# Optimization experiments

Hardware: AMD Instinct MI355X
Metric: run time of the kernel (lower is better)

## Reference

```python
import jax, jax.numpy as jnp
import numpy as np

WIDTH = 1024
NH = 16
HD = 64
MBS = 16
B = 4
L = 2048
BASE_LR = 1.0
EPS = 1e-6


def gelu_tanh(x):
    return jax.nn.gelu(x, approximate=True)


def gelu_bwd(x):
    t = jnp.tanh(0.79788456 * x * (1 + 0.044715 * x * x))
    return 0.5 * x * ((1 - t * t) * (0.79788456 + 0.1070322243 * x * x)) + 0.5 * (1 + t)


def ln_fwd(x, g, b):
    mu = x.mean(-1, keepdims=True)
    var = ((x - mu) ** 2).mean(-1, keepdims=True)
    return g * ((x - mu) * jax.lax.rsqrt(var + EPS)) + b


def ln_l2_bwd(x, tgt, g, b):
    # grad of 0.5*||LN(x)-tgt||^2 wrt x
    mu = x.mean(-1, keepdims=True)
    var = ((x - mu) ** 2).mean(-1, keepdims=True)
    std = jnp.sqrt(var + EPS)
    xh = (x - mu) / std
    gx = (g * xh + b - tgt) * g
    return (gx - gx.mean(-1, keepdims=True) - xh * (gx * xh).mean(-1, keepdims=True)) / std


def adapter_forward(hidden_states, Wq, Wk, Wv, Wo, Wg, lr_w, lr_b,
                    learnable_token_idx, norm_w, norm_b, W1, b1, W2, b2,
                    post_w, post_b):
    Bb, Ll, width = hidden_states.shape
    nh, hd = norm_w.shape
    mbs = learnable_token_idx.shape[0]
    nc = Ll // mbs  # L chosen divisible by mini_batch_size

    def split_heads(x):  # [B,L,width] -> [B,nh,nc,mbs,hd]
        return x.reshape(Bb, Ll, nh, hd).transpose(0, 2, 1, 3).reshape(Bb, nh, nc, mbs, hd)

    XQ = split_heads(hidden_states @ Wq.T)
    XK = split_heads(hidden_states @ Wk.T)
    XV = split_heads(hidden_states @ Wv.T)

    # eta: learnable per-token lr gate (get_eta)
    X = hidden_states.reshape(Bb, nc, mbs, width)
    lr = jnp.einsum('bnkc,hdc->bhnkd', X, lr_w) + lr_b.reshape(1, nh, 1, 1, 1)
    lr = jax.nn.sigmoid(lr).transpose(0, 1, 2, 4, 3)  # [B,nh,nc,1,mbs]
    lr_eta = BASE_LR * lr / hd
    token_idx = jnp.clip(1.0 / jnp.arange(1, mbs + 1, dtype=hidden_states.dtype)
                         + learnable_token_idx, 0.0, None)
    token_eta = token_idx.reshape(1, 1, 1, mbs, 1)
    eta = token_eta * lr_eta  # [B,nh,nc,mbs,mbs]

    tril = jnp.tril(jnp.ones((mbs, mbs), dtype=hidden_states.dtype))
    lnw = norm_w.reshape(nh, 1, hd)
    lnb = norm_b.reshape(nh, 1, hd)

    def step(carry, xs):
        W1s, b1s, W2s, b2s = carry  # [B,nh,hd,4hd], [B,nh,1,4hd], [B,nh,4hd,hd], [B,nh,1,hd]
        XQm, XKm, XVm, etam = xs    # [B,nh,mbs,hd] x3, [B,nh,mbs,mbs]
        X1 = XKm
        Z1 = X1 @ W1s + b1s
        X2 = gelu_tanh(Z1)
        Z2 = X2 @ W2s + b2s
        gZ2 = ln_l2_bwd(Z2, XVm - XKm, lnw, lnb)
        gZ1 = (gZ2 @ jnp.swapaxes(W2s, -1, -2)) * gelu_bwd(Z1)
        eta_tril = etam * tril
        Attn1 = tril * (XQm @ jnp.swapaxes(X1, -1, -2))
        b1_bar = b1s - eta_tril @ gZ1
        Z1_bar = XQm @ W1s - (etam * Attn1) @ gZ1 + b1_bar
        X2_bar = gelu_tanh(Z1_bar)
        Attn2 = tril * (X2_bar @ jnp.swapaxes(X2, -1, -2))
        b2_bar = b2s - eta_tril @ gZ2
        Z2_bar = X2_bar @ W2s - (etam * Attn2) @ gZ2 + b2_bar
        last = etam[:, :, -1, :, None]  # [B,nh,mbs,1]
        W1n = W1s - jnp.swapaxes(last * X1, -1, -2) @ gZ1
        b1n = b1s - (last * gZ1).sum(-2, keepdims=True)
        W2n = W2s - jnp.swapaxes(last * X2, -1, -2) @ gZ2
        b2n = b2s - (last * gZ2).sum(-2, keepdims=True)
        XQW = XQm + ln_fwd(Z2_bar, lnw, lnb)
        return (W1n, b1n, W2n, b2n), XQW

    carry0 = (jnp.broadcast_to(W1, (Bb,) + W1.shape),
              jnp.broadcast_to(b1, (Bb,) + b1.shape),
              jnp.broadcast_to(W2, (Bb,) + W2.shape),
              jnp.broadcast_to(b2, (Bb,) + b2.shape))
    xs = tuple(jnp.moveaxis(t, 2, 0) for t in (XQ, XK, XV, eta))
    _, XQW = jax.lax.scan(step, carry0, xs)  # [nc,B,nh,mbs,hd]
    out = XQW.transpose(1, 0, 3, 2, 4).reshape(Bb, Ll, width)

    # post_norm (LayerNorm eps=1e-6)
    out = ln_fwd(out, post_w, post_b)
    # gate
    out = gelu_tanh(hidden_states @ Wg.T) * out
    # o_proj
    return out @ Wo.T


def setup_inputs():
    key = jax.random.key(0)
    ks = jax.random.split(key, 10)
    n = lambda k, s: jax.random.normal(k, s, dtype=jnp.float32) * 0.02
    return {
        'hidden_states': jax.random.normal(ks[0], (B, L, WIDTH), dtype=jnp.float32),
        'Wq': n(ks[1], (WIDTH, WIDTH)),
        'Wk': n(ks[2], (WIDTH, WIDTH)),
        'Wv': n(ks[3], (WIDTH, WIDTH)),
        'Wo': n(ks[4], (WIDTH, WIDTH)),
        'Wg': n(ks[5], (WIDTH, WIDTH)),
        'lr_w': n(ks[6], (NH, 1, WIDTH)),
        'lr_b': jnp.zeros((NH, 1), jnp.float32),
        'learnable_token_idx': jnp.zeros((MBS,), jnp.float32),
        'norm_w': jnp.ones((NH, HD), jnp.float32),
        'norm_b': jnp.zeros((NH, HD), jnp.float32),
        'W1': n(ks[7], (NH, HD, 4 * HD)),
        'b1': jnp.zeros((NH, 1, 4 * HD), jnp.float32),
        'W2': n(ks[8], (NH, 4 * HD, HD)),
        'b2': jnp.zeros((NH, 1, HD), jnp.float32),
        'post_w': jnp.ones((WIDTH,), jnp.float32),
        'post_b': jnp.zeros((WIDTH,), jnp.float32),
    }


def reference(hidden_states, Wq, Wk, Wv, Wo, Wg, lr_w, lr_b, learnable_token_idx,
              norm_w, norm_b, W1, b1, W2, b2, post_w, post_b):
    return adapter_forward(hidden_states, Wq, Wk, Wv, Wo, Wg, lr_w, lr_b,
                           learnable_token_idx, norm_w, norm_b, W1, b1, W2, b2,
                           post_w, post_b)
```

## Files before the change

### kernel.cpp

```cpp
#include <hip/hip_runtime.h>

#define WIDTH 1024
#define MBSZ 16
#define LLL 2048
#define NCHUNK 128

typedef __attribute__((ext_vector_type(4))) float f32x4;
typedef __attribute__((ext_vector_type(2))) float f32x2;
typedef __attribute__((ext_vector_type(8))) short short8;
typedef __attribute__((ext_vector_type(4))) short short4v;
typedef __attribute__((ext_vector_type(2))) unsigned u32x2;
typedef __attribute__((ext_vector_type(4))) unsigned u32x4;

#define MFMA16(a, b, c) __builtin_amdgcn_mfma_f32_16x16x32_bf16((a), (b), (c), 0, 0, 0)

__device__ __forceinline__ short f2bf(float f) {
  unsigned u = __float_as_uint(f);
  u = (u + 0x7FFFu + ((u >> 16) & 1u)) >> 16;
  return (short)u;
}
__device__ __forceinline__ float bf2f(short s) {
  return __uint_as_float(((unsigned)(unsigned short)s) << 16);
}
__device__ __forceinline__ unsigned cvt_pk(float lo, float hi) {
  unsigned r;
  asm("v_cvt_pk_bf16_f32 %0, %1, %2" : "=v"(r) : "v"(lo), "v"(hi));
  return r;
}
__device__ __forceinline__ float fast_e2u(float x) {
  return __builtin_amdgcn_exp2f(x * (2.30220776f + 0.10294322f * x * x));
}
__device__ __forceinline__ float gelu_f(float x) {
  float e = fast_e2u(x);
  return x * (1.0f - __builtin_amdgcn_rcpf(e + 1.0f));
}
__device__ __forceinline__ float gelu_bwd_f(float x) {
  float e = fast_e2u(x);
  float r = __builtin_amdgcn_rcpf(e + 1.0f);
  return 2.0f * x * r * (1.0f - r) * (0.79788456f + 0.1070322243f * x * x) + (1.0f - r);
}
__device__ __forceinline__ int w2row(int d) { return d * 264 + (d >> 3) * 24; }

__global__ __launch_bounds__(256) void cvt_kernel(const float* __restrict__ hs,
                                                  const float* __restrict__ Wq,
                                                  const float* __restrict__ Wk,
                                                  const float* __restrict__ Wv,
                                                  const float* __restrict__ Wg,
                                                  const float* __restrict__ Wo,
                                                  short* __restrict__ dst) {
  const long idx = ((long)blockIdx.x * 256 + threadIdx.x) * 8;
  if (idx >= 13631488L) return;
  const float* src;
  long off;
  if (idx < 8388608L)       { src = hs; off = idx; }
  else if (idx < 9437184L)  { src = Wq; off = idx - 8388608L; }
  else if (idx < 10485760L) { src = Wk; off = idx - 9437184L; }
  else if (idx < 11534336L) { src = Wv; off = idx - 10485760L; }
  else if (idx < 12582912L) { src = Wg; off = idx - 11534336L; }
  else                      { src = Wo; off = idx - 12582912L; }
  const f32x4 a = *(const f32x4*)(src + off);
  const f32x4 b = *(const f32x4*)(src + off + 4);
  u32x4 o;
  o[0] = cvt_pk(a[0], a[1]); o[1] = cvt_pk(a[2], a[3]);
  o[2] = cvt_pk(b[0], b[1]); o[3] = cvt_pk(b[2], b[3]);
  *(u32x4*)(dst + idx) = o;
}

template <int OUTBF>
__global__ __launch_bounds__(256) void gemm_bt_b(const short* __restrict__ A,
                                                 const short* __restrict__ W,
                                                 float* __restrict__ C,
                                                 short* __restrict__ Cb) {
  __shared__ __align__(16) short sA[64][40];
  __shared__ __align__(16) short sB[64][40];
  const int tid = threadIdx.x;
  const int m0 = blockIdx.x * 64, n0 = blockIdx.y * 64;
  const int srow = tid >> 2, sk = (tid & 3) * 8;
  const int wv = tid >> 6, ln = tid & 63;
  const int fr = ln & 15, kh = (ln >> 4) * 8;
  f32x4 acc[4];
#pragma unroll
  for (int s = 0; s < 4; ++s) acc[s] = (f32x4){0.f, 0.f, 0.f, 0.f};
  const short* ga = A + (long)(m0 + srow) * 1024 + sk;
  const short* gw = W + (long)(n0 + srow) * 1024 + sk;
  for (int k0 = 0; k0 < 1024; k0 += 32) {
    const short8 a8 = *(const short8*)(ga + k0);
    const short8 w8 = *(const short8*)(gw + k0);
    *(short8*)&sA[srow][sk] = a8;
    *(short8*)&sB[srow][sk] = w8;
    __syncthreads();
    short8 af = *(const short8*)&sA[wv * 16 + fr][kh];
#pragma unroll
    for (int s = 0; s < 4; ++s) {
      short8 bf8 = *(const short8*)&sB[s * 16 + fr][kh];
      acc[s] = MFMA16(af, bf8, acc[s]);
    }
    __syncthreads();
  }
  const int orow = m0 + wv * 16 + (ln >> 4) * 4;
#pragma unroll
  for (int s = 0; s < 4; ++s)
#pragma unroll
    for (int q = 0; q < 4; ++q) {
      if (OUTBF)
        Cb[(long)(orow + q) * 1024 + n0 + s * 16 + fr] = f2bf(acc[s][q]);
      else
        C[(long)(orow + q) * 1024 + n0 + s * 16 + fr] = acc[s][q];
    }
}

__global__ __launch_bounds__(256) void lr_kernel(const float* __restrict__ hs,
                                                 const float* __restrict__ lrw,
                                                 const float* __restrict__ lrb,
                                                 float* __restrict__ out) {
  __shared__ __align__(16) float row[1024];
  const int t = blockIdx.x, tid = threadIdx.x;
  *(f32x4*)&row[tid * 4] = *(const f32x4*)&hs[(long)t * 1024 + tid * 4];
  __syncthreads();
  const int hh = tid >> 4, j = tid & 15;
  const float* wrow = lrw + hh * 1024;
  float s = 0.f;
#pragma unroll 4
  for (int m = 0; m < 16; ++m) {
    const int c = j * 4 + m * 64;
    f32x4 x = *(const f32x4*)&row[c];
    f32x4 w = *(const f32x4*)&wrow[c];
    s += x[0] * w[0] + x[1] * w[1] + x[2] * w[2] + x[3] * w[3];
  }
#pragma unroll
  for (int o = 8; o; o >>= 1) s += __shfl_xor(s, o, 16);
  if (j == 0) {
    const float v = s + lrb[hh];
    const float sg = 1.f / (1.f + expf(-v));
    const int b = t >> 11, tr = t & 2047;
    out[((b << 4) + hh) * 2048 + tr] = sg * (1.f / 64.f);
  }
}

__global__ __launch_bounds__(512, 2) void scan_kernel(
    float* __restrict__ Qb, const float* __restrict__ Kb, const float* __restrict__ Vb,
    const float* __restrict__ LRb, const float* __restrict__ lti,
    const float* __restrict__ nw, const float* __restrict__ nb,
    const float* __restrict__ W1in, const float* __restrict__ b1in,
    const float* __restrict__ W2in, const float* __restrict__ b2in) {
  __shared__ __align__(16) short sW1b[256 * 72];
  __shared__ __align__(16) short sW2dp[64 * 264 + 192];
  __shared__ __align__(16) short la1T[64 * 24];
  __shared__ __align__(16) short la2T[256 * 24];
  __shared__ __align__(16) short sX1b[16 * 72];
  __shared__ __align__(16) short sXQb[16 * 72];
  __shared__ __align__(16) float sXQf[16 * 68];
  __shared__ __align__(16) float sTg[16 * 72];
  __shared__ __align__(16) short sX2b[16 * 264];
  __shared__ __align__(16) short sXbb[16 * 264];
  __shared__ __align__(16) short sG1c[256 * 24];
  __shared__ __align__(16) short sG2b[16 * 72];
  __shared__ __align__(16) short sG2c[64 * 24];
  __shared__ __align__(16) float sZ2f[16 * 68];
  __shared__ __align__(16) short sC1b[16 * 24];
  __shared__ __align__(16) short sC2b[16 * 24];
  __shared__ __align__(16) float sB1[256];
  __shared__ __align__(16) float sB2[64];
  __shared__ float sLr[16];
  __shared__ float sTok[16];
  __shared__ __align__(16) float sLnw[64];
  __shared__ __align__(16) float sLnb[64];

  const int bh = blockIdx.x, b = bh >> 4, h = bh & 15;
  const int tid = threadIdx.x;
  const int w = tid >> 6, ln = tid & 63;
  const int fr = ln & 15, half = ln >> 4, hk = half * 8;
  const int nt0 = 2 * w;

  float w1m[8][4], w2m[8][4];
#pragma unroll
  for (int r = 0; r < 8; ++r) {
    const int T = w * 8 + r, dt = T >> 4, pt = T & 15;
#pragma unroll
    for (int qq = 0; qq < 4; ++qq) {
      w1m[r][qq] = W1in[h * 16384 + (dt * 16 + half * 4 + qq) * 256 + pt * 16 + fr];
      w2m[r][qq] = W2in[h * 16384 + (pt * 16 + half * 4 + qq) * 64 + dt * 16 + fr];
    }
  }
  for (int e = tid; e < 16384; e += 512) {
    {
      const int d = e >> 8, p = e & 255;
      sW1b[p * 72 + d] = f2bf(W1in[h * 16384 + e]);
    }
    {
      const int p = e >> 6, d = e & 63;
      sW2dp[w2row(d) + (p ^ (((d >> 3) & 3) << 3))] = f2bf(W2in[h * 16384 + e]);
    }
  }
  if (tid < 256) sB1[tid] = b1in[h * 256 + tid];
  if (tid < 64) { sB2[tid] = b2in[h * 64 + tid]; sLnw[tid] = nw[h * 64 + tid]; sLnb[tid] = nb[h * 64 + tid]; }
  if (tid < 16) sTok[tid] = fmaxf(1.0f / (float)(tid + 1) + lti[tid], 0.0f);

  const f32x4 zf4 = (f32x4){0.f, 0.f, 0.f, 0.f};
  short8 zs8;
#pragma unroll
  for (int j = 0; j < 8; ++j) zs8[j] = 0;

  const int pf_i = tid >> 5;
  const int pf_d = (tid & 31) * 2;
  f32x2 pk, pq, pv;
  float plr = 0.f;
  {
    const long a0 = ((long)(b * LLL + pf_i)) * WIDTH + h * 64 + pf_d;
    pk = *(const f32x2*)&Kb[a0];
    pq = *(const f32x2*)&Qb[a0];
    pv = *(const f32x2*)&Vb[a0];
    if (tid < 16) plr = LRb[(long)bh * 2048 + tid];
  }

  for (int n = 0; n < NCHUNK; ++n) {
    const long gbase = ((long)(b * LLL + n * MBSZ)) * WIDTH + h * 64;

    {
      *(unsigned*)&sX1b[pf_i * 72 + pf_d] = cvt_pk(pk[0], pk[1]);
      *(unsigned*)&sXQb[pf_i * 72 + pf_d] = cvt_pk(pq[0], pq[1]);
      sXQf[pf_i * 68 + pf_d] = pq[0];
      sXQf[pf_i * 68 + pf_d + 1] = pq[1];
      sTg[pf_i * 72 + pf_d] = pv[0] - pk[0];
      sTg[pf_i * 72 + pf_d + 1] = pv[1] - pk[1];
      if (tid < 16) sLr[tid] = plr;
    }
    __syncthreads();

    short8 aX1[2], aXQ[2];
    aX1[0] = *(const short8*)&sX1b[fr * 72 + hk];
    aX1[1] = *(const short8*)&sX1b[fr * 72 + 32 + hk];
    aXQ[0] = *(const short8*)&sXQb[fr * 72 + hk];
    aXQ[1] = *(const short8*)&sXQb[fr * 72 + 32 + hk];
    f32x4 z1[2], q1[2];
    float b1p[2];
#pragma unroll
    for (int t = 0; t < 2; ++t) {
      const int p = (nt0 + t) * 16 + fr;
      z1[t] = zf4; q1[t] = zf4;
#pragma unroll
      for (int ks = 0; ks < 2; ++ks) {
        short8 bw = *(const short8*)&sW1b[p * 72 + ks * 32 + hk];
        z1[t] = MFMA16(aX1[ks], bw, z1[t]);
        q1[t] = MFMA16(aXQ[ks], bw, q1[t]);
      }
      b1p[t] = sB1[p];
#pragma unroll
      for (int qq = 0; qq < 4; ++qq) {
        z1[t][qq] += b1p[t];
        sX2b[(half * 4 + qq) * 264 + p] = f2bf(gelu_f(z1[t][qq]));
      }
    }
    {
      const float tok15 = sTok[15];
      const int d = tid >> 3, j0 = (tid & 7) * 2;
      const float v0 = bf2f(sX1b[j0 * 72 + d]) * (tok15 * sLr[j0]);
      const float v1 = bf2f(sX1b[(j0 + 1) * 72 + d]) * (tok15 * sLr[j0 + 1]);
      *(unsigned*)&la1T[d * 24 + j0] = cvt_pk(v0, v1);
    }
    if (w == 0) {
      f32x4 c = MFMA16(aXQ[0], aX1[0], zf4);
      c = MFMA16(aXQ[1], aX1[1], c);
#pragma unroll
      for (int qq = 0; qq < 4; ++qq) {
        const int i = half * 4 + qq, j = fr;
        sC1b[i * 24 + j] = f2bf((i >= j) ? sTok[i] * sLr[j] * (c[qq] + 1.0f) : 0.0f);
      }
    }
    __syncthreads();

    float bb2old = 0.f;
    if (w < 4) {
      const int d = w * 16 + fr;
      const int sw = ((d >> 3) & 3) << 3;
      const int rb = w2row(d);
      f32x4 za = zf4, zb = zf4;
#pragma unroll
      for (int ks = 0; ks < 4; ++ks) {
        short8 a = *(const short8*)&sX2b[fr * 264 + ks * 32 + hk];
        short8 bfr = *(const short8*)&sW2dp[rb + ((ks * 32 + hk) ^ sw)];
        za = MFMA16(a, bfr, za);
      }
#pragma unroll
      for (int ks = 4; ks < 8; ++ks) {
        short8 a = *(const short8*)&sX2b[fr * 264 + ks * 32 + hk];
        short8 bfr = *(const short8*)&sW2dp[rb + ((ks * 32 + hk) ^ sw)];
        zb = MFMA16(a, bfr, zb);
      }
      bb2old = sB2[d];
#pragma unroll
      for (int qq = 0; qq < 4; ++qq)
        sZ2f[(half * 4 + qq) * 68 + d] = za[qq] + zb[qq] + bb2old;
    }
    __syncthreads();

    if (tid < 256) {
      const int i = tid >> 4, j4 = tid & 15;
      const f32x4 z = *(const f32x4*)&sZ2f[i * 68 + j4 * 4];
      float s1 = z[0] + z[1] + z[2] + z[3];
      float s2 = z[0] * z[0] + z[1] * z[1] + z[2] * z[2] + z[3] * z[3];
#pragma unroll
      for (int o = 8; o; o >>= 1) { s1 += __shfl_xor(s1, o, 16); s2 += __shfl_xor(s2, o, 16); }
      const float mu = s1 * (1.f / 64.f);
      const float rstd = rsqrtf(s2 * (1.f / 64.f) - mu * mu + 1e-6f);
      const f32x4 g = *(const f32x4*)&sLnw[j4 * 4];
      const f32x4 bb = *(const f32x4*)&sLnb[j4 * 4];
      const f32x4 tg = *(const f32x4*)&sTg[i * 72 + j4 * 4];
      f32x4 xh, gx;
      float a1 = 0.f, a2 = 0.f;
#pragma unroll
      for (int e = 0; e < 4; ++e) {
        xh[e] = (z[e] - mu) * rstd;
        gx[e] = (g[e] * xh[e] + bb[e] - tg[e]) * g[e];
        a1 += gx[e]; a2 += gx[e] * xh[e];
      }
#pragma unroll
      for (int o = 8; o; o >>= 1) { a1 += __shfl_xor(a1, o, 16); a2 += __shfl_xor(a2, o, 16); }
      const float m1 = a1 * (1.f / 64.f), m2 = a2 * (1.f / 64.f);
      float o4[4];
#pragma unroll
      for (int e = 0; e < 4; ++e) o4[e] = (gx[e] - m1 - xh[e] * m2) * rstd;
      const unsigned lo = cvt_pk(o4[0], o4[1]);
      const unsigned hi = cvt_pk(o4[2], o4[3]);
      *(u32x2*)&sG2b[i * 72 + j4 * 4] = (u32x2){lo, hi};
      sG2c[(j4 * 4 + 0) * 24 + i] = (short)lo;
      sG2c[(j4 * 4 + 1) * 24 + i] = (short)(lo >> 16);
      sG2c[(j4 * 4 + 2) * 24 + i] = (short)hi;
      sG2c[(j4 * 4 + 3) * 24 + i] = (short)(hi >> 16);
    } else {
      const int pp = tid - 256;
      const float tok15 = sTok[15];
      unsigned uu[8];
#pragma unroll
      for (int jp = 0; jp < 8; ++jp) {
        const float v0 = bf2f(sX2b[(2 * jp) * 264 + pp]) * (tok15 * sLr[2 * jp]);
        const float v1 = bf2f(sX2b[(2 * jp + 1) * 264 + pp]) * (tok15 * sLr[2 * jp + 1]);
        uu[jp] = cvt_pk(v0, v1);
      }
      *(u32x4*)&la2T[pp * 24] = (u32x4){uu[0], uu[1], uu[2], uu[3]};
      *(u32x4*)&la2T[pp * 24 + 8] = (u32x4){uu[4], uu[5], uu[6], uu[7]};
    }
    __syncthreads();

    {
      short8 aG2[2];
      aG2[0] = *(const short8*)&sG2b[fr * 72 + hk];
      aG2[1] = *(const short8*)&sG2b[fr * 72 + 32 + hk];
#pragma unroll
      for (int t = 0; t < 2; ++t) {
        const int p = (nt0 + t) * 16 + fr;
        f32x4 g = zf4;
#pragma unroll
        for (int ks = 0; ks < 2; ++ks) {
          const int dg = ks * 32 + hk;
          const int rb = w2row(dg) + (p ^ (((dg >> 3) & 3) << 3));
          short8 bw;
#pragma unroll
          for (int jj = 0; jj < 8; ++jj) bw[jj] = sW2dp[rb + jj * 264];
          g = MFMA16(aG2[ks], bw, g);
        }
        const unsigned lo = cvt_pk(g[0] * gelu_bwd_f(z1[t][0]), g[1] * gelu_bwd_f(z1[t][1]));
        const unsigned hi = cvt_pk(g[2] * gelu_bwd_f(z1[t][2]), g[3] * gelu_bwd_f(z1[t][3]));
        *(u32x2*)&sG1c[p * 24 + half * 4] = (u32x2){lo, hi};
      }
    }
    if (tid < 64) {
      float s = 0.f;
#pragma unroll
      for (int j = 0; j < 16; ++j) s += sLr[j] * bf2f(sG2c[tid * 24 + j]);
      sB2[tid] -= sTok[15] * s;
    }
    __syncthreads();

    {
      short8 ac = zs8;
      if (half < 2) ac = *(const short8*)&sC1b[fr * 24 + hk];
#pragma unroll
      for (int t = 0; t < 2; ++t) {
        const int p = (nt0 + t) * 16 + fr;
        short8 bg = zs8;
        if (half < 2) bg = *(const short8*)&sG1c[p * 24 + hk];
        f32x4 corr = MFMA16(ac, bg, zf4);
#pragma unroll
        for (int qq = 0; qq < 4; ++qq)
          sXbb[(half * 4 + qq) * 264 + p] = f2bf(gelu_f(q1[t][qq] + b1p[t] - corr[qq]));
      }
    }
    {
#pragma unroll
      for (int r = 0; r < 8; ++r) {
        const int T = w * 8 + r, dt = T >> 4, pt = T & 15;
        short8 af = zs8, bg = zs8;
        if (half < 2) {
          af = *(const short8*)&la1T[(dt * 16 + fr) * 24 + hk];
          bg = *(const short8*)&sG1c[(pt * 16 + fr) * 24 + hk];
        }
        f32x4 dl = MFMA16(af, bg, zf4);
        const int pp = pt * 16 + fr, d0 = dt * 16 + half * 4;
        w1m[r][0] -= dl[0]; w1m[r][1] -= dl[1]; w1m[r][2] -= dl[2]; w1m[r][3] -= dl[3];
        const unsigned lo = cvt_pk(w1m[r][0], w1m[r][1]);
        const unsigned hi = cvt_pk(w1m[r][2], w1m[r][3]);
        *(u32x2*)&sW1b[pp * 72 + d0] = (u32x2){lo, hi};
      }
    }
    if (tid < 256) {
      float s = 0.f;
#pragma unroll
      for (int j = 0; j < 16; ++j) s += sLr[j] * bf2f(sG1c[tid * 24 + j]);
      sB1[tid] -= sTok[15] * s;
    }
    __syncthreads();

    {
      const int nn = (n + 1 < NCHUNK) ? n + 1 : n;
      const long a1 = ((long)(b * LLL + nn * MBSZ + pf_i)) * WIDTH + h * 64 + pf_d;
      pk = *(const f32x2*)&Kb[a1];
      pq = *(const f32x2*)&Qb[a1];
      pv = *(const f32x2*)&Vb[a1];
      if (tid < 16) plr = LRb[(long)bh * 2048 + nn * MBSZ + tid];
    }
    f32x4 zbar = zf4;
    if (w < 4) {
      const int d = w * 16 + fr;
      const int sw = ((d >> 3) & 3) << 3;
      const int rb = w2row(d);
      f32x4 za = zf4, zb = zf4;
#pragma unroll
      for (int ks = 0; ks < 4; ++ks) {
        short8 a = *(const short8*)&sXbb[fr * 264 + ks * 32 + hk];
        short8 bfr = *(const short8*)&sW2dp[rb + ((ks * 32 + hk) ^ sw)];
        za = MFMA16(a, bfr, za);
      }
#pragma unroll
      for (int ks = 4; ks < 8; ++ks) {
        short8 a = *(const short8*)&sXbb[fr * 264 + ks * 32 + hk];
        short8 bfr = *(const short8*)&sW2dp[rb + ((ks * 32 + hk) ^ sw)];
        zb = MFMA16(a, bfr, zb);
      }
      zbar[0] = za[0] + zb[0]; zbar[1] = za[1] + zb[1];
      zbar[2] = za[2] + zb[2]; zbar[3] = za[3] + zb[3];
    } else if (w == 4) {
      f32x4 c = zf4;
#pragma unroll
      for (int ks = 0; ks < 8; ++ks) {
        short8 a = *(const short8*)&sXbb[fr * 264 + ks * 32 + hk];
        short8 bx = *(const short8*)&sX2b[fr * 264 + ks * 32 + hk];
        c = MFMA16(a, bx, c);
      }
#pragma unroll
      for (int qq = 0; qq < 4; ++qq) {
        const int i = half * 4 + qq, j = fr;
        sC2b[i * 24 + j] = f2bf((i >= j) ? sTok[i] * sLr[j] * (c[qq] + 1.0f) : 0.0f);
      }
    }
    __syncthreads();

    if (w < 4) {
      const int d = w * 16 + fr;
      short8 ac = zs8, bg = zs8;
      if (half < 2) {
        ac = *(const short8*)&sC2b[fr * 24 + hk];
        bg = *(const short8*)&sG2c[d * 24 + hk];
      }
      f32x4 corr = MFMA16(ac, bg, zf4);
#pragma unroll
      for (int qq = 0; qq < 4; ++qq)
        sZ2f[(half * 4 + qq) * 68 + d] = zbar[qq] + bb2old - corr[qq];
    }
    {
#pragma unroll
      for (int r = 0; r < 8; ++r) {
        const int T = w * 8 + r, pt = T & 15, dt = T >> 4;
        short8 af = zs8, bg = zs8;
        if (half < 2) {
          af = *(const short8*)&la2T[(pt * 16 + fr) * 24 + hk];
          bg = *(const short8*)&sG2c[(dt * 16 + fr) * 24 + hk];
        }
        f32x4 dl = MFMA16(af, bg, zf4);
        const int dd = dt * 16 + fr;
        const int swp = ((dd >> 3) & 3) << 3;
        const int p0 = pt * 16 + half * 4;
        w2m[r][0] -= dl[0]; w2m[r][1] -= dl[1]; w2m[r][2] -= dl[2]; w2m[r][3] -= dl[3];
        const unsigned lo = cvt_pk(w2m[r][0], w2m[r][1]);
        const unsigned hi = cvt_pk(w2m[r][2], w2m[r][3]);
        *(u32x2*)&sW2dp[w2row(dd) + (p0 ^ swp)] = (u32x2){lo, hi};
      }
    }
    __syncthreads();

    if (tid < 256) {
      const int i = tid >> 4, j4 = tid & 15;
      const f32x4 z = *(const f32x4*)&sZ2f[i * 68 + j4 * 4];
      float s1 = z[0] + z[1] + z[2] + z[3];
      float s2 = z[0] * z[0] + z[1] * z[1] + z[2] * z[2] + z[3] * z[3];
#pragma unroll
      for (int o = 8; o; o >>= 1) { s1 += __shfl_xor(s1, o, 16); s2 += __shfl_xor(s2, o, 16); }
      const float mu = s1 * (1.f / 64.f);
      const float rstd = rsqrtf(s2 * (1.f / 64.f) - mu * mu + 1e-6f);
      const f32x4 g = *(const f32x4*)&sLnw[j4 * 4];
      const f32x4 bb = *(const f32x4*)&sLnb[j4 * 4];
      const f32x4 xq = *(const f32x4*)&sXQf[i * 68 + j4 * 4];
      f32x4 o4;
#pragma unroll
      for (int e = 0; e < 4; ++e) o4[e] = xq[e] + g[e] * ((z[e] - mu) * rstd) + bb[e];
      *(f32x4*)&Qb[gbase + (long)i * WIDTH + j4 * 4] = o4;
    }
    __syncthreads();
  }
}

__global__ __launch_bounds__(256) void epi_kernel(const float* __restrict__ X,
                                                  const short* __restrict__ G,
                                                  const float* __restrict__ pw,
                                                  const float* __restrict__ pb,
                                                  short* __restrict__ T) {
  __shared__ float red[8];
  const int t = blockIdx.x, tid = threadIdx.x;
  const long base = (long)t * 1024 + tid * 4;
  f32x4 x = *(const f32x4*)&X[base];
  float s1 = x[0] + x[1] + x[2] + x[3];
  float s2 = x[0] * x[0] + x[1] * x[1] + x[2] * x[2] + x[3] * x[3];
#pragma unroll
  for (int o = 32; o; o >>= 1) { s1 += __shfl_xor(s1, o, 64); s2 += __shfl_xor(s2, o, 64); }
  const int wv = tid >> 6, ln = tid & 63;
  if (ln == 0) { red[wv] = s1; red[4 + wv] = s2; }
  __syncthreads();
  s1 = red[0] + red[1] + red[2] + red[3];
  s2 = red[4] + red[5] + red[6] + red[7];
  const float mu = s1 * (1.f / 1024.f);
  const float rstd = rsqrtf(s2 * (1.f / 1024.f) - mu * mu + 1e-6f);
  const short4v g4 = *(const short4v*)&G[base];
  f32x4 w = *(const f32x4*)&pw[tid * 4];
  f32x4 bb = *(const f32x4*)&pb[tid * 4];
  float o4[4];
#pragma unroll
  for (int e = 0; e < 4; ++e) {
    float y = w[e] * ((x[e] - mu) * rstd) + bb[e];
    o4[e] = gelu_f(bf2f(g4[e])) * y;
  }
  *(u32x2*)&T[base] = (u32x2){cvt_pk(o4[0], o4[1]), cvt_pk(o4[2], o4[3])};
}

extern "C" void kernel_launch(void* const* d_in, const int* in_sizes, int n_in,
                              void* d_out, int out_size, void* d_ws, size_t ws_size,
                              hipStream_t stream) {
  const float* hs  = (const float*)d_in[0];
  const float* Wq  = (const float*)d_in[1];
  const float* Wk  = (const float*)d_in[2];
  const float* Wv  = (const float*)d_in[3];
  const float* Wo  = (const float*)d_in[4];
  const float* Wg  = (const float*)d_in[5];
  const float* lrw = (const float*)d_in[6];
  const float* lrb = (const float*)d_in[7];
  const float* lti = (const float*)d_in[8];
  const float* nw  = (const float*)d_in[9];
  const float* nb  = (const float*)d_in[10];
  const float* W1  = (const float*)d_in[11];
  const float* b1  = (const float*)d_in[12];
  const float* W2  = (const float*)d_in[13];
  const float* b2  = (const float*)d_in[14];
  const float* pw  = (const float*)d_in[15];
  const float* pb  = (const float*)d_in[16];
  float* out = (float*)d_out;
  float* ws = (float*)d_ws;

  float* Qb  = ws;
  float* Kb  = ws + 8388608;
  float* Vb  = ws + 16777216;
  float* LRb = ws + 25165824;
  short* hsb = (short*)(ws + 25296896);
  short* Wqb = hsb + 8388608;
  short* Wkb = Wqb + 1048576;
  short* Wvb = Wkb + 1048576;
  short* Wgb = Wvb + 1048576;
  short* Wob = Wgb + 1048576;
  short* Tb  = (short*)Kb;
  short* Gbb = (short*)Vb;

  dim3 gg(128, 16);
  cvt_kernel<<<6656, 256, 0, stream>>>(hs, Wq, Wk, Wv, Wg, Wo, hsb);
  gemm_bt_b<0><<<gg, 256, 0, stream>>>(hsb, Wqb, Qb, nullptr);
  gemm_bt_b<0><<<gg, 256, 0, stream>>>(hsb, Wkb, Kb, nullptr);
  gemm_bt_b<0><<<gg, 256, 0, stream>>>(hsb, Wvb, Vb, nullptr);
  lr_kernel<<<8192, 256, 0, stream>>>(hs, lrw, lrb, LRb);
  scan_kernel<<<64, 512, 0, stream>>>(Qb, Kb, Vb, LRb, lti, nw, nb, W1, b1, W2, b2);
  gemm_bt_b<1><<<gg, 256, 0, stream>>>(hsb, Wgb, nullptr, Gbb);
  epi_kernel<<<8192, 256, 0, stream>>>(Qb, Gbb, pw, pb, Tb);
  gemm_bt_b<0><<<gg, 256, 0, stream>>>(Tb, Wob, out, nullptr);
}
```

Baseline: 990.9 us.

## Double-buffer chunk inputs, split W2 matmul across all waves, fuse b1 update

Chunk inputs (K, Q, V-K target, lr) now go into double-buffered LDS as bf16. The next chunk's staging moves to the end of the previous iteration, which removes one barrier per chunk. The Z2 forward matmul is split by K across all 8 waves into two partial buffers that are summed in the LN step. The b1 gradient reduction and the C1 correction are fused into the G1 computation using shuffles, which removes another barrier. Keeping the residual Q and the target in bf16 instead of fp32 lowers precision and could change accuracy.

```diff
diff --git a/kernel.cpp b/kernel.cpp
--- a/kernel.cpp
+++ b/kernel.cpp
@@ -147,21 +147,22 @@
   __shared__ __align__(16) short sW2dp[64 * 264 + 192];
   __shared__ __align__(16) short la1T[64 * 24];
   __shared__ __align__(16) short la2T[256 * 24];
-  __shared__ __align__(16) short sX1b[16 * 72];
-  __shared__ __align__(16) short sXQb[16 * 72];
-  __shared__ __align__(16) float sXQf[16 * 68];
-  __shared__ __align__(16) float sTg[16 * 72];
+  __shared__ __align__(16) short sX1b[2][16 * 72];
+  __shared__ __align__(16) short sXQb[2][16 * 72];
+  __shared__ __align__(16) short sTgb[2][16 * 72];
   __shared__ __align__(16) short sX2b[16 * 264];
   __shared__ __align__(16) short sXbb[16 * 264];
   __shared__ __align__(16) short sG1c[256 * 24];
   __shared__ __align__(16) short sG2b[16 * 72];
   __shared__ __align__(16) short sG2c[64 * 24];
+  __shared__ __align__(16) float sZ2p0[16 * 68];
+  __shared__ __align__(16) float sZ2p1[16 * 68];
   __shared__ __align__(16) float sZ2f[16 * 68];
   __shared__ __align__(16) short sC1b[16 * 24];
   __shared__ __align__(16) short sC2b[16 * 24];
   __shared__ __align__(16) float sB1[256];
   __shared__ __align__(16) float sB2[64];
-  __shared__ float sLr[16];
+  __shared__ float sLr2[2][16];
   __shared__ float sTok[16];
   __shared__ __align__(16) float sLnw[64];
   __shared__ __align__(16) float sLnb[64];
@@ -211,27 +212,21 @@
     pq = *(const f32x2*)&Qb[a0];
     pv = *(const f32x2*)&Vb[a0];
     if (tid < 16) plr = LRb[(long)bh * 2048 + tid];
-  }
+    *(unsigned*)&sX1b[0][pf_i * 72 + pf_d] = cvt_pk(pk[0], pk[1]);
+    *(unsigned*)&sXQb[0][pf_i * 72 + pf_d] = cvt_pk(pq[0], pq[1]);
+    *(unsigned*)&sTgb[0][pf_i * 72 + pf_d] = cvt_pk(pv[0] - pk[0], pv[1] - pk[1]);
+    if (tid < 16) sLr2[0][tid] = plr;
+  }
+  __syncthreads();
 
   for (int n = 0; n < NCHUNK; ++n) {
-    const long gbase = ((long)(b * LLL + n * MBSZ)) * WIDTH + h * 64;
-
-    {
-      *(unsigned*)&sX1b[pf_i * 72 + pf_d] = cvt_pk(pk[0], pk[1]);
-      *(unsigned*)&sXQb[pf_i * 72 + pf_d] = cvt_pk(pq[0], pq[1]);
-      sXQf[pf_i * 68 + pf_d] = pq[0];
-      sXQf[pf_i * 68 + pf_d + 1] = pq[1];
-      sTg[pf_i * 72 + pf_d] = pv[0] - pk[0];
-      sTg[pf_i * 72 + pf_d + 1] = pv[1] - pk[1];
-      if (tid < 16) sLr[tid] = plr;
-    }
-    __syncthreads();
+    const int cb = n & 1;
 
     short8 aX1[2], aXQ[2];
-    aX1[0] = *(const short8*)&sX1b[fr * 72 + hk];
-    aX1[1] = *(const short8*)&sX1b[fr * 72 + 32 + hk];
-    aXQ[0] = *(const short8*)&sXQb[fr * 72 + hk];
-    aXQ[1] = *(const short8*)&sXQb[fr * 72 + 32 + hk];
+    aX1[0] = *(const short8*)&sX1b[cb][fr * 72 + hk];
+    aX1[1] = *(const short8*)&sX1b[cb][fr * 72 + 32 + hk];
+    aXQ[0] = *(const short8*)&sXQb[cb][fr * 72 + hk];
+    aXQ[1] = *(const short8*)&sXQb[cb][fr * 72 + 32 + hk];
     f32x4 z1[2], q1[2];
     float b1p[2];
 #pragma unroll
@@ -254,8 +249,8 @@
     {
       const float tok15 = sTok[15];
       const int d = tid >> 3, j0 = (tid & 7) * 2;
-      const float v0 = bf2f(sX1b[j0 * 72 + d]) * (tok15 * sLr[j0]);
-      const float v1 = bf2f(sX1b[(j0 + 1) * 72 + d]) * (tok15 * sLr[j0 + 1]);
+      const float v0 = bf2f(sX1b[cb][j0 * 72 + d]) * (tok15 * sLr2[cb][j0]);
+      const float v1 = bf2f(sX1b[cb][(j0 + 1) * 72 + d]) * (tok15 * sLr2[cb][j0 + 1]);
       *(unsigned*)&la1T[d * 24 + j0] = cvt_pk(v0, v1);
     }
     if (w == 0) {
@@ -264,39 +259,46 @@
 #pragma unroll
       for (int qq = 0; qq < 4; ++qq) {
         const int i = half * 4 + qq, j = fr;
-        sC1b[i * 24 + j] = f2bf((i >= j) ? sTok[i] * sLr[j] * (c[qq] + 1.0f) : 0.0f);
+        sC1b[i * 24 + j] = f2bf((i >= j) ? sTok[i] * sLr2[cb][j] * (c[qq] + 1.0f) : 0.0f);
       }
     }
     __syncthreads();
 
     float bb2old = 0.f;
-    if (w < 4) {
-      const int d = w * 16 + fr;
+    {
+      const int dt = w & 3, k2 = w >> 2;
+      const int d = dt * 16 + fr;
       const int sw = ((d >> 3) & 3) << 3;
       const int rb = w2row(d);
       f32x4 za = zf4, zb = zf4;
 #pragma unroll
-      for (int ks = 0; ks < 4; ++ks) {
+      for (int ks = k2 * 4; ks < k2 * 4 + 2; ++ks) {
         short8 a = *(const short8*)&sX2b[fr * 264 + ks * 32 + hk];
         short8 bfr = *(const short8*)&sW2dp[rb + ((ks * 32 + hk) ^ sw)];
         za = MFMA16(a, bfr, za);
       }
 #pragma unroll
-      for (int ks = 4; ks < 8; ++ks) {
+      for (int ks = k2 * 4 + 2; ks < k2 * 4 + 4; ++ks) {
         short8 a = *(const short8*)&sX2b[fr * 264 + ks * 32 + hk];
         short8 bfr = *(const short8*)&sW2dp[rb + ((ks * 32 + hk) ^ sw)];
         zb = MFMA16(a, bfr, zb);
       }
-      bb2old = sB2[d];
+      float* dst = k2 ? sZ2p1 : sZ2p0;
 #pragma unroll
       for (int qq = 0; qq < 4; ++qq)
-        sZ2f[(half * 4 + qq) * 68 + d] = za[qq] + zb[qq] + bb2old;
+        dst[(half * 4 + qq) * 68 + d] = za[qq] + zb[qq];
+      if (w < 4) bb2old = sB2[w * 16 + fr];
     }
     __syncthreads();
 
     if (tid < 256) {
       const int i = tid >> 4, j4 = tid & 15;
-      const f32x4 z = *(const f32x4*)&sZ2f[i * 68 + j4 * 4];
+      const f32x4 zp0 = *(const f32x4*)&sZ2p0[i * 68 + j4 * 4];
+      const f32x4 zp1 = *(const f32x4*)&sZ2p1[i * 68 + j4 * 4];
+      const f32x4 b2v = *(const f32x4*)&sB2[j4 * 4];
+      f32x4 z;
+#pragma unroll
+      for (int e = 0; e < 4; ++e) z[e] = zp0[e] + zp1[e] + b2v[e];
       float s1 = z[0] + z[1] + z[2] + z[3];
       float s2 = z[0] * z[0] + z[1] * z[1] + z[2] * z[2] + z[3] * z[3];
 #pragma unroll
@@ -305,13 +307,13 @@
       const float rstd = rsqrtf(s2 * (1.f / 64.f) - mu * mu + 1e-6f);
       const f32x4 g = *(const f32x4*)&sLnw[j4 * 4];
       const f32x4 bb = *(const f32x4*)&sLnb[j4 * 4];
-      const f32x4 tg = *(const f32x4*)&sTg[i * 72 + j4 * 4];
+      const short4v t4 = *(const short4v*)&sTgb[cb][i * 72 + j4 * 4];
       f32x4 xh, gx;
       float a1 = 0.f, a2 = 0.f;
 #pragma unroll
       for (int e = 0; e < 4; ++e) {
         xh[e] = (z[e] - mu) * rstd;
-        gx[e] = (g[e] * xh[e] + bb[e] - tg[e]) * g[e];
+        gx[e] = (g[e] * xh[e] + bb[e] - bf2f(t4[e])) * g[e];
         a1 += gx[e]; a2 += gx[e] * xh[e];
       }
 #pragma unroll
@@ -333,8 +335,8 @@
       unsigned uu[8];
 #pragma unroll
       for (int jp = 0; jp < 8; ++jp) {
-        const float v0 = bf2f(sX2b[(2 * jp) * 264 + pp]) * (tok15 * sLr[2 * jp]);
-        const float v1 = bf2f(sX2b[(2 * jp + 1) * 264 + pp]) * (tok15 * sLr[2 * jp + 1]);
+        const float v0 = bf2f(sX2b[(2 * jp) * 264 + pp]) * (tok15 * sLr2[cb][2 * jp]);
+        const float v1 = bf2f(sX2b[(2 * jp + 1) * 264 + pp]) * (tok15 * sLr2[cb][2 * jp + 1]);
         uu[jp] = cvt_pk(v0, v1);
       }
       *(u32x4*)&la2T[pp * 24] = (u32x4){uu[0], uu[1], uu[2], uu[3]};
@@ -346,6 +348,11 @@
       short8 aG2[2];
       aG2[0] = *(const short8*)&sG2b[fr * 72 + hk];
       aG2[1] = *(const short8*)&sG2b[fr * 72 + 32 + hk];
+      const float tok15 = sTok[15];
+      float lrq[4];
+#pragma unroll
+      for (int qq = 0; qq < 4; ++qq) lrq[qq] = sLr2[cb][half * 4 + qq];
+      unsigned lo_t[2], hi_t[2];
 #pragma unroll
       for (int t = 0; t < 2; ++t) {
         const int p = (nt0 + t) * 16 + fr;
@@ -353,38 +360,59 @@
 #pragma unroll
         for (int ks = 0; ks < 2; ++ks) {
           const int dg = ks * 32 + hk;
-          const int rb = w2row(dg) + (p ^ (((dg >> 3) & 3) << 3));
+          const int rb2 = w2row(dg) + (p ^ (((dg >> 3) & 3) << 3));
           short8 bw;
 #pragma unroll
-          for (int jj = 0; jj < 8; ++jj) bw[jj] = sW2dp[rb + jj * 264];
+          for (int jj = 0; jj < 8; ++jj) bw[jj] = sW2dp[rb2 + jj * 264];
           g = MFMA16(aG2[ks], bw, g);
         }
-        const unsigned lo = cvt_pk(g[0] * gelu_bwd_f(z1[t][0]), g[1] * gelu_bwd_f(z1[t][1]));
-        const unsigned hi = cvt_pk(g[2] * gelu_bwd_f(z1[t][2]), g[3] * gelu_bwd_f(z1[t][3]));
-        *(u32x2*)&sG1c[p * 24 + half * 4] = (u32x2){lo, hi};
+        const float g0 = g[0] * gelu_bwd_f(z1[t][0]);
+        const float g1v = g[1] * gelu_bwd_f(z1[t][1]);
+        const float g2v = g[2] * gelu_bwd_f(z1[t][2]);
+        const float g3v = g[3] * gelu_bwd_f(z1[t][3]);
+        lo_t[t] = cvt_pk(g0, g1v);
+        hi_t[t] = cvt_pk(g2v, g3v);
+        *(u32x2*)&sG1c[p * 24 + half * 4] = (u32x2){lo_t[t], hi_t[t]};
+        float s = lrq[0] * g0 + lrq[1] * g1v + lrq[2] * g2v + lrq[3] * g3v;
+        s += __shfl_xor(s, 16, 64);
+        s += __shfl_xor(s, 32, 64);
+        if (half == 0) sB1[p] -= tok15 * s;
+      }
+      short8 ac = zs8;
+      if (half < 2) ac = *(const short8*)&sC1b[fr * 24 + hk];
+      const int src01 = fr + ((half == 1) ? 32 : 0);
+      const int src23 = src01 + 16;
+#pragma unroll
+      for (int t = 0; t < 2; ++t) {
+        unsigned a0 = (unsigned)__shfl((int)lo_t[t], src01, 64);
+        unsigned a1 = (unsigned)__shfl((int)hi_t[t], src01, 64);
+        unsigned a2 = (unsigned)__shfl((int)lo_t[t], src23, 64);
+        unsigned a3 = (unsigned)__shfl((int)hi_t[t], src23, 64);
+        if (half >= 2) { a0 = 0; a1 = 0; a2 = 0; a3 = 0; }
+        const u32x4 bgu = (u32x4){a0, a1, a2, a3};
+        const short8 bg = __builtin_bit_cast(short8, bgu);
+        f32x4 corr = MFMA16(ac, bg, zf4);
+        const int p = (nt0 + t) * 16 + fr;
+#pragma unroll
+        for (int qq = 0; qq < 4; ++qq)
+          sXbb[(half * 4 + qq) * 264 + p] = f2bf(gelu_f(q1[t][qq] + b1p[t] - corr[qq]));
       }
     }
     if (tid < 64) {
       float s = 0.f;
 #pragma unroll
-      for (int j = 0; j < 16; ++j) s += sLr[j] * bf2f(sG2c[tid * 24 + j]);
+      for (int j = 0; j < 16; ++j) s += sLr2[cb][j] * bf2f(sG2c[tid * 24 + j]);
       sB2[tid] -= sTok[15] * s;
     }
     __syncthreads();
 
     {
-      short8 ac = zs8;
-      if (half < 2) ac = *(const short8*)&sC1b[fr * 24 + hk];
-#pragma unroll
-      for (int t = 0; t < 2; ++t) {
-        const int p = (nt0 + t) * 16 + fr;
-        short8 bg = zs8;
-        if (half < 2) bg = *(const short8*)&sG1c[p * 24 + hk];
-        f32x4 corr = MFMA16(ac, bg, zf4);
-#pragma unroll
-        for (int qq = 0; qq < 4; ++qq)
-          sXbb[(half * 4 + qq) * 264 + p] = f2bf(gelu_f(q1[t][qq] + b1p[t] - corr[qq]));
-      }
+      const int nn = (n + 1 < NCHUNK) ? n + 1 : n;
+      const long a1 = ((long)(b * LLL + nn * MBSZ + pf_i)) * WIDTH + h * 64 + pf_d;
+      pk = *(const f32x2*)&Kb[a1];
+      pq = *(const f32x2*)&Qb[a1];
+      pv = *(const f32x2*)&Vb[a1];
+      if (tid < 16) plr = LRb[(long)bh * 2048 + nn * MBSZ + tid];
     }
     {
 #pragma unroll
@@ -403,22 +431,6 @@
         *(u32x2*)&sW1b[pp * 72 + d0] = (u32x2){lo, hi};
       }
     }
-    if (tid < 256) {
-      float s = 0.f;
-#pragma unroll
-      for (int j = 0; j < 16; ++j) s += sLr[j] * bf2f(sG1c[tid * 24 + j]);
-      sB1[tid] -= sTok[15] * s;
-    }
-    __syncthreads();
-
-    {
-      const int nn = (n + 1 < NCHUNK) ? n + 1 : n;
-      const long a1 = ((long)(b * LLL + nn * MBSZ + pf_i)) * WIDTH + h * 64 + pf_d;
-      pk = *(const f32x2*)&Kb[a1];
-      pq = *(const f32x2*)&Qb[a1];
-      pv = *(const f32x2*)&Vb[a1];
-      if (tid < 16) plr = LRb[(long)bh * 2048 + nn * MBSZ + tid];
-    }
     f32x4 zbar = zf4;
     if (w < 4) {
       const int d = w * 16 + fr;
@@ -450,7 +462,7 @@
 #pragma unroll
       for (int qq = 0; qq < 4; ++qq) {
         const int i = half * 4 + qq, j = fr;
-        sC2b[i * 24 + j] = f2bf((i >= j) ? sTok[i] * sLr[j] * (c[qq] + 1.0f) : 0.0f);
+        sC2b[i * 24 + j] = f2bf((i >= j) ? sTok[i] * sLr2[cb][j] * (c[qq] + 1.0f) : 0.0f);
       }
     }
     __syncthreads();
@@ -489,6 +501,7 @@
     __syncthreads();
 
     if (tid < 256) {
+      const long gbase = ((long)(b * LLL + n * MBSZ)) * WIDTH + h * 64;
       const int i = tid >> 4, j4 = tid & 15;
       const f32x4 z = *(const f32x4*)&sZ2f[i * 68 + j4 * 4];
       float s1 = z[0] + z[1] + z[2] + z[3];
@@ -499,11 +512,19 @@
       const float rstd = rsqrtf(s2 * (1.f / 64.f) - mu * mu + 1e-6f);
       const f32x4 g = *(const f32x4*)&sLnw[j4 * 4];
       const f32x4 bb = *(const f32x4*)&sLnb[j4 * 4];
-      const f32x4 xq = *(const f32x4*)&sXQf[i * 68 + j4 * 4];
+      const short4v xq4 = *(const short4v*)&sXQb[cb][i * 72 + j4 * 4];
       f32x4 o4;
 #pragma unroll
-      for (int e = 0; e < 4; ++e) o4[e] = xq[e] + g[e] * ((z[e] - mu) * rstd) + bb[e];
+      for (int e = 0; e < 4; ++e)
+        o4[e] = bf2f(xq4[e]) + g[e] * ((z[e] - mu) * rstd) + bb[e];
       *(f32x4*)&Qb[gbase + (long)i * WIDTH + j4 * 4] = o4;
+    }
+    {
+      const int nb2 = cb ^ 1;
+      *(unsigned*)&sX1b[nb2][pf_i * 72 + pf_d] = cvt_pk(pk[0], pk[1]);
+      *(unsigned*)&sXQb[nb2][pf_i * 72 + pf_d] = cvt_pk(pq[0], pq[1]);
+      *(unsigned*)&sTgb[nb2][pf_i * 72 + pf_d] = cvt_pk(pv[0] - pk[0], pv[1] - pk[1]);
+      if (tid < 16) sLr2[nb2][tid] = plr;
     }
     __syncthreads();
   }
```

Result: slower. 1.017 ms (+2.7%).

## Double scan kernel block to 1024 threads and split-K the W2 matmuls

Applied to the files above, without the earlier changes.

The sequential scan kernel now runs 1024 threads (16 waves) per batch-head block instead of 512, so each wave owns half as many W1/W2 register tiles and one 16-column slice of the W1 forward/backward work. The two Z2 matmuls over the 256-wide hidden dim are split across 8 waves with split-K, writing partial sums to two new shared buffers that are reduced later. This targets the per-chunk latency of the serial 128-step loop, which has only 64 blocks and so leaves most CUs idle. In exchange it adds shared-memory traffic for the partial sums, heavier barrier cost with more waves, and register pressure under the 1024-thread launch bound.

```diff
diff --git a/kernel.cpp b/kernel.cpp
--- a/kernel.cpp
+++ b/kernel.cpp
@@ -137,7 +137,7 @@
   }
 }
 
-__global__ __launch_bounds__(512, 2) void scan_kernel(
+__global__ __launch_bounds__(1024) void scan_kernel(
     float* __restrict__ Qb, const float* __restrict__ Kb, const float* __restrict__ Vb,
     const float* __restrict__ LRb, const float* __restrict__ lti,
     const float* __restrict__ nw, const float* __restrict__ nb,
@@ -156,6 +156,8 @@
   __shared__ __align__(16) short sG1c[256 * 24];
   __shared__ __align__(16) short sG2b[16 * 72];
   __shared__ __align__(16) short sG2c[64 * 24];
+  __shared__ __align__(16) float sZ2p0[16 * 68];
+  __shared__ __align__(16) float sZ2p1[16 * 68];
   __shared__ __align__(16) float sZ2f[16 * 68];
   __shared__ __align__(16) short sC1b[16 * 24];
   __shared__ __align__(16) short sC2b[16 * 24];
@@ -170,19 +172,18 @@
   const int tid = threadIdx.x;
   const int w = tid >> 6, ln = tid & 63;
   const int fr = ln & 15, half = ln >> 4, hk = half * 8;
-  const int nt0 = 2 * w;
-
-  float w1m[8][4], w2m[8][4];
-#pragma unroll
-  for (int r = 0; r < 8; ++r) {
-    const int T = w * 8 + r, dt = T >> 4, pt = T & 15;
+
+  float w1m[4][4], w2m[4][4];
+#pragma unroll
+  for (int r = 0; r < 4; ++r) {
+    const int T = w * 4 + r, dt = T >> 4, pt = T & 15;
 #pragma unroll
     for (int qq = 0; qq < 4; ++qq) {
       w1m[r][qq] = W1in[h * 16384 + (dt * 16 + half * 4 + qq) * 256 + pt * 16 + fr];
       w2m[r][qq] = W2in[h * 16384 + (pt * 16 + half * 4 + qq) * 64 + dt * 16 + fr];
     }
   }
-  for (int e = tid; e < 16384; e += 512) {
+  for (int e = tid; e < 16384; e += 1024) {
     {
       const int d = e >> 8, p = e & 255;
       sW1b[p * 72 + d] = f2bf(W1in[h * 16384 + e]);
@@ -205,7 +206,7 @@
   const int pf_d = (tid & 31) * 2;
   f32x2 pk, pq, pv;
   float plr = 0.f;
-  {
+  if (tid < 512) {
     const long a0 = ((long)(b * LLL + pf_i)) * WIDTH + h * 64 + pf_d;
     pk = *(const f32x2*)&Kb[a0];
     pq = *(const f32x2*)&Qb[a0];
@@ -216,7 +217,7 @@
   for (int n = 0; n < NCHUNK; ++n) {
     const long gbase = ((long)(b * LLL + n * MBSZ)) * WIDTH + h * 64;
 
-    {
+    if (tid < 512) {
       *(unsigned*)&sX1b[pf_i * 72 + pf_d] = cvt_pk(pk[0], pk[1]);
       *(unsigned*)&sXQb[pf_i * 72 + pf_d] = cvt_pk(pq[0], pq[1]);
       sXQf[pf_i * 68 + pf_d] = pq[0];
@@ -232,26 +233,25 @@
     aX1[1] = *(const short8*)&sX1b[fr * 72 + 32 + hk];
     aXQ[0] = *(const short8*)&sXQb[fr * 72 + hk];
     aXQ[1] = *(const short8*)&sXQb[fr * 72 + 32 + hk];
-    f32x4 z1[2], q1[2];
-    float b1p[2];
-#pragma unroll
-    for (int t = 0; t < 2; ++t) {
-      const int p = (nt0 + t) * 16 + fr;
-      z1[t] = zf4; q1[t] = zf4;
+    f32x4 z1, q1;
+    float b1p;
+    {
+      const int p = w * 16 + fr;
+      z1 = zf4; q1 = zf4;
 #pragma unroll
       for (int ks = 0; ks < 2; ++ks) {
         short8 bw = *(const short8*)&sW1b[p * 72 + ks * 32 + hk];
-        z1[t] = MFMA16(aX1[ks], bw, z1[t]);
-        q1[t] = MFMA16(aXQ[ks], bw, q1[t]);
-      }
-      b1p[t] = sB1[p];
+        z1 = MFMA16(aX1[ks], bw, z1);
+        q1 = MFMA16(aXQ[ks], bw, q1);
+      }
+      b1p = sB1[p];
 #pragma unroll
       for (int qq = 0; qq < 4; ++qq) {
-        z1[t][qq] += b1p[t];
-        sX2b[(half * 4 + qq) * 264 + p] = f2bf(gelu_f(z1[t][qq]));
-      }
-    }
-    {
+        z1[qq] += b1p;
+        sX2b[(half * 4 + qq) * 264 + p] = f2bf(gelu_f(z1[qq]));
+      }
+    }
+    if (tid < 512) {
       const float tok15 = sTok[15];
       const int d = tid >> 3, j0 = (tid & 7) * 2;
       const float v0 = bf2f(sX1b[j0 * 72 + d]) * (tok15 * sLr[j0]);
@@ -270,33 +270,40 @@
     __syncthreads();
 
     float bb2old = 0.f;
-    if (w < 4) {
-      const int d = w * 16 + fr;
+    if (w < 8) {
+      const int dt = w & 3, k2 = w >> 2;
+      const int d = dt * 16 + fr;
       const int sw = ((d >> 3) & 3) << 3;
       const int rb = w2row(d);
       f32x4 za = zf4, zb = zf4;
 #pragma unroll
-      for (int ks = 0; ks < 4; ++ks) {
+      for (int ks = k2 * 4; ks < k2 * 4 + 2; ++ks) {
         short8 a = *(const short8*)&sX2b[fr * 264 + ks * 32 + hk];
         short8 bfr = *(const short8*)&sW2dp[rb + ((ks * 32 + hk) ^ sw)];
         za = MFMA16(a, bfr, za);
       }
 #pragma unroll
-      for (int ks = 4; ks < 8; ++ks) {
+      for (int ks = k2 * 4 + 2; ks < k2 * 4 + 4; ++ks) {
         short8 a = *(const short8*)&sX2b[fr * 264 + ks * 32 + hk];
         short8 bfr = *(const short8*)&sW2dp[rb + ((ks * 32 + hk) ^ sw)];
         zb = MFMA16(a, bfr, zb);
       }
-      bb2old = sB2[d];
+      float* dst = k2 ? sZ2p1 : sZ2p0;
 #pragma unroll
       for (int qq = 0; qq < 4; ++qq)
-        sZ2f[(half * 4 + qq) * 68 + d] = za[qq] + zb[qq] + bb2old;
+        dst[(half * 4 + qq) * 68 + d] = za[qq] + zb[qq];
+      if (w < 4) bb2old = sB2[w * 16 + fr];
     }
     __syncthreads();
 
     if (tid < 256) {
       const int i = tid >> 4, j4 = tid & 15;
-      const f32x4 z = *(const f32x4*)&sZ2f[i * 68 + j4 * 4];
+      const f32x4 zp0 = *(const f32x4*)&sZ2p0[i * 68 + j4 * 4];
+      const f32x4 zp1 = *(const f32x4*)&sZ2p1[i * 68 + j4 * 4];
+      const f32x4 b2v = *(const f32x4*)&sB2[j4 * 4];
+      f32x4 z;
+#pragma unroll
+      for (int e = 0; e < 4; ++e) z[e] = zp0[e] + zp1[e] + b2v[e];
       float s1 = z[0] + z[1] + z[2] + z[3];
       float s2 = z[0] * z[0] + z[1] * z[1] + z[2] * z[2] + z[3] * z[3];
 #pragma unroll
@@ -327,7 +334,7 @@
       sG2c[(j4 * 4 + 1) * 24 + i] = (short)(lo >> 16);
       sG2c[(j4 * 4 + 2) * 24 + i] = (short)hi;
       sG2c[(j4 * 4 + 3) * 24 + i] = (short)(hi >> 16);
-    } else {
+    } else if (tid < 512) {
       const int pp = tid - 256;
       const float tok15 = sTok[15];
       unsigned uu[8];
@@ -346,23 +353,20 @@
       short8 aG2[2];
       aG2[0] = *(const short8*)&sG2b[fr * 72 + hk];
       aG2[1] = *(const short8*)&sG2b[fr * 72 + 32 + hk];
-#pragma unroll
-      for (int t = 0; t < 2; ++t) {
-        const int p = (nt0 + t) * 16 + fr;
-        f32x4 g = zf4;
-#pragma unroll
-        for (int ks = 0; ks < 2; ++ks) {
-          const int dg = ks * 32 + hk;
-          const int rb = w2row(dg) + (p ^ (((dg >> 3) & 3) << 3));
-          short8 bw;
-#pragma unroll
-          for (int jj = 0; jj < 8; ++jj) bw[jj] = sW2dp[rb + jj * 264];
-          g = MFMA16(aG2[ks], bw, g);
-        }
-        const unsigned lo = cvt_pk(g[0] * gelu_bwd_f(z1[t][0]), g[1] * gelu_bwd_f(z1[t][1]));
-        const unsigned hi = cvt_pk(g[2] * gelu_bwd_f(z1[t][2]), g[3] * gelu_bwd_f(z1[t][3]));
-        *(u32x2*)&sG1c[p * 24 + half * 4] = (u32x2){lo, hi};
-      }
+      const int p = w * 16 + fr;
+      f32x4 g = zf4;
+#pragma unroll
+      for (int ks = 0; ks < 2; ++ks) {
+        const int dg = ks * 32 + hk;
+        const int rb2 = w2row(dg) + (p ^ (((dg >> 3) & 3) << 3));
+        short8 bw;
+#pragma unroll
+        for (int jj = 0; jj < 8; ++jj) bw[jj] = sW2dp[rb2 + jj * 264];
+        g = MFMA16(aG2[ks], bw, g);
+      }
+      const unsigned lo = cvt_pk(g[0] * gelu_bwd_f(z1[0]), g[1] * gelu_bwd_f(z1[1]));
+      const unsigned hi = cvt_pk(g[2] * gelu_bwd_f(z1[2]), g[3] * gelu_bwd_f(z1[3]));
+      *(u32x2*)&sG1c[p * 24 + half * 4] = (u32x2){lo, hi};
     }
     if (tid < 64) {
       float s = 0.f;
@@ -375,21 +379,18 @@
     {
       short8 ac = zs8;
       if (half < 2) ac = *(const short8*)&sC1b[fr * 24 + hk];
-#pragma unroll
-      for (int t = 0; t < 2; ++t) {
-        const int p = (nt0 + t) * 16 + fr;
-        short8 bg = zs8;
-        if (half < 2) bg = *(const short8*)&sG1c[p * 24 + hk];
-        f32x4 corr = MFMA16(ac, bg, zf4);
-#pragma unroll
-        for (int qq = 0; qq < 4; ++qq)
-          sXbb[(half * 4 + qq) * 264 + p] = f2bf(gelu_f(q1[t][qq] + b1p[t] - corr[qq]));
-      }
-    }
-    {
-#pragma unroll
-      for (int r = 0; r < 8; ++r) {
-        const int T = w * 8 + r, dt = T >> 4, pt = T & 15;
+      const int p = w * 16 + fr;
+      short8 bg = zs8;
+      if (half < 2) bg = *(const short8*)&sG1c[p * 24 + hk];
+      f32x4 corr = MFMA16(ac, bg, zf4);
+#pragma unroll
+      for (int qq = 0; qq < 4; ++qq)
+        sXbb[(half * 4 + qq) * 264 + p] = f2bf(gelu_f(q1[qq] + b1p - corr[qq]));
+    }
+    {
+#pragma unroll
+      for (int r = 0; r < 4; ++r) {
+        const int T = w * 4 + r, dt = T >> 4, pt = T & 15;
         short8 af = zs8, bg = zs8;
         if (half < 2) {
           af = *(const short8*)&la1T[(dt * 16 + fr) * 24 + hk];
@@ -411,7 +412,7 @@
     }
     __syncthreads();
 
-    {
+    if (tid < 512) {
       const int nn = (n + 1 < NCHUNK) ? n + 1 : n;
       const long a1 = ((long)(b * LLL + nn * MBSZ + pf_i)) * WIDTH + h * 64 + pf_d;
       pk = *(const f32x2*)&Kb[a1];
@@ -419,27 +420,29 @@
       pv = *(const f32x2*)&Vb[a1];
       if (tid < 16) plr = LRb[(long)bh * 2048 + nn * MBSZ + tid];
     }
-    f32x4 zbar = zf4;
-    if (w < 4) {
-      const int d = w * 16 + fr;
+    if (w < 8) {
+      const int dt = w & 3, k2 = w >> 2;
+      const int d = dt * 16 + fr;
       const int sw = ((d >> 3) & 3) << 3;
       const int rb = w2row(d);
       f32x4 za = zf4, zb = zf4;
 #pragma unroll
-      for (int ks = 0; ks < 4; ++ks) {
+      for (int ks = k2 * 4; ks < k2 * 4 + 2; ++ks) {
         short8 a = *(const short8*)&sXbb[fr * 264 + ks * 32 + hk];
         short8 bfr = *(const short8*)&sW2dp[rb + ((ks * 32 + hk) ^ sw)];
         za = MFMA16(a, bfr, za);
       }
 #pragma unroll
-      for (int ks = 4; ks < 8; ++ks) {
+      for (int ks = k2 * 4 + 2; ks < k2 * 4 + 4; ++ks) {
         short8 a = *(const short8*)&sXbb[fr * 264 + ks * 32 + hk];
         short8 bfr = *(const short8*)&sW2dp[rb + ((ks * 32 + hk) ^ sw)];
         zb = MFMA16(a, bfr, zb);
       }
-      zbar[0] = za[0] + zb[0]; zbar[1] = za[1] + zb[1];
-      zbar[2] = za[2] + zb[2]; zbar[3] = za[3] + zb[3];
-    } else if (w == 4) {
+      float* dst = k2 ? sZ2p1 : sZ2p0;
+#pragma unroll
+      for (int qq = 0; qq < 4; ++qq)
+        dst[(half * 4 + qq) * 68 + d] = za[qq] + zb[qq];
+    } else if (w == 8) {
       f32x4 c = zf4;
 #pragma unroll
       for (int ks = 0; ks < 8; ++ks) {
@@ -464,13 +467,15 @@
       }
       f32x4 corr = MFMA16(ac, bg, zf4);
 #pragma unroll
-      for (int qq = 0; qq < 4; ++qq)
-        sZ2f[(half * 4 + qq) * 68 + d] = zbar[qq] + bb2old - corr[qq];
-    }
-    {
-#pragma unroll
-      for (int r = 0; r < 8; ++r) {
-        const int T = w * 8 + r, pt = T & 15, dt = T >> 4;
+      for (int qq = 0; qq < 4; ++qq) {
+        const int row = (half * 4 + qq) * 68 + d;
+        sZ2f[row] = sZ2p0[row] + sZ2p1[row] + bb2old - corr[qq];
+      }
+    }
+    {
+#pragma unroll
+      for (int r = 0; r < 4; ++r) {
+        const int T = w * 4 + r, pt = T & 15, dt = T >> 4;
         short8 af = zs8, bg = zs8;
         if (half < 2) {
           af = *(const short8*)&la2T[(pt * 16 + fr) * 24 + hk];
@@ -583,7 +588,7 @@
   gemm_bt_b<0><<<gg, 256, 0, stream>>>(hsb, Wkb, Kb, nullptr);
   gemm_bt_b<0><<<gg, 256, 0, stream>>>(hsb, Wvb, Vb, nullptr);
   lr_kernel<<<8192, 256, 0, stream>>>(hs, lrw, lrb, LRb);
-  scan_kernel<<<64, 512, 0, stream>>>(Qb, Kb, Vb, LRb, lti, nw, nb, W1, b1, W2, b2);
+  scan_kernel<<<64, 1024, 0, stream>>>(Qb, Kb, Vb, LRb, lti, nw, nb, W1, b1, W2, b2);
   gemm_bt_b<1><<<gg, 256, 0, stream>>>(hsb, Wgb, nullptr, Gbb);
   epi_kernel<<<8192, 256, 0, stream>>>(Qb, Gbb, pw, pb, Tb);
   gemm_bt_b<0><<<gg, 256, 0, stream>>>(Tb, Wob, out, nullptr);
```

New measurement: 1.384 ms. +39.7%, slower.
